# Performance work log

Hardware: AMD Instinct MI355X
Metric: run time of the kernel (lower is better)

## Reference

```python
import jax, jax.numpy as jnp
import numpy as np

B, S, E = 2, 2048, 1024
H, HKV = 16, 4
D = E // H          # head_dim = 64
REP = H // HKV      # kv repeat factor = 4


def setup_inputs() -> dict:
    key = jax.random.key(0)
    ks = jax.random.split(key, 9)
    std = 0.02
    x = jax.random.normal(ks[0], (B, S, E), dtype=jnp.float32)
    # causal mask: True means masked (upper triangle, strictly above diagonal)
    mask = jnp.triu(jnp.ones((S, S), dtype=bool), k=1)
    wq_w = jax.random.normal(ks[1], (E, E), dtype=jnp.float32) * std
    wq_b = jax.random.normal(ks[2], (E,), dtype=jnp.float32) * std
    wk_w = jax.random.normal(ks[3], (HKV * D, E), dtype=jnp.float32) * std
    wk_b = jax.random.normal(ks[4], (HKV * D,), dtype=jnp.float32) * std
    wv_w = jax.random.normal(ks[5], (HKV * D, E), dtype=jnp.float32) * std
    wv_b = jax.random.normal(ks[6], (HKV * D,), dtype=jnp.float32) * std
    wo_w = jax.random.normal(ks[7], (E, E), dtype=jnp.float32) * std
    wo_b = jax.random.normal(ks[8], (E,), dtype=jnp.float32) * std
    return {"x": x, "mask": mask, "wq_w": wq_w, "wq_b": wq_b,
            "wk_w": wk_w, "wk_b": wk_b, "wv_w": wv_w, "wv_b": wv_b,
            "wo_w": wo_w, "wo_b": wo_b}


def reference(x, mask, wq_w, wq_b, wk_w, wk_b, wv_w, wv_b, wo_w, wo_b):
    b, s, e = x.shape
    # projections (torch Linear: x @ W.T + b)
    q = x @ wq_w.T + wq_b                       # [B,S,E]
    k = x @ wk_w.T + wk_b                       # [B,S,HKV*D]
    v = x @ wv_w.T + wv_b
    # q grouped by kv head: [B, HKV, REP, S, D]; k/v: [B, HKV, S, D]
    q = q.reshape(b, s, HKV, REP, D).transpose(0, 2, 3, 1, 4)
    k = k.reshape(b, s, HKV, D).transpose(0, 2, 1, 3)
    v = v.reshape(b, s, HKV, D).transpose(0, 2, 1, 3)
    scale = D ** (-0.5)
    # scores [B, HKV, REP, Sq, Skv] -- same math as physical repeat_kv
    scores = jnp.einsum('bgrsd,bgtd->bgrst', q, k) * scale
    scores = jnp.where(mask, -jnp.inf, scores)
    w = jax.nn.softmax(scores, axis=-1)
    ctx = jnp.einsum('bgrst,bgtd->bgrsd', w, v)  # [B,HKV,REP,S,D]
    ctx = ctx.transpose(0, 3, 1, 2, 4).reshape(b, s, e)
    return ctx @ wo_w.T + wo_b
```

## Files before the change

### kernel.cpp

```cpp
#include <hip/hip_runtime.h>


typedef __attribute__((ext_vector_type(8))) short bh8;
typedef __attribute__((ext_vector_type(4))) short sh4;
typedef __attribute__((ext_vector_type(4))) float fv4;

#define MFMA16 __builtin_amdgcn_mfma_f32_16x16x32_bf16

static __device__ __forceinline__ float fast_exp2(float x) {
  return __builtin_amdgcn_exp2f(x);
}
static __device__ __forceinline__ unsigned short f2bf(float f) {
  unsigned int u; __builtin_memcpy(&u, &f, 4);
  u += 0x7fffu + ((u >> 16) & 1u);
  return (unsigned short)(u >> 16);
}
static __device__ __forceinline__ unsigned int pack2(float a, float b) {
  return (unsigned int)(unsigned short)f2bf(a) |
         ((unsigned int)(unsigned short)f2bf(b) << 16);
}
static __device__ __forceinline__ void gload16(const short* g, short* l) {
  __builtin_amdgcn_global_load_lds(
      (const __attribute__((address_space(1))) void*)g,
      (__attribute__((address_space(3))) void*)l, 16, 0, 0);
}

static __device__ __forceinline__ bh8 pshuf(const float* p, int quad, int l16) {
  unsigned int u01 = pack2(p[0], p[1]);
  unsigned int u23 = pack2(p[2], p[3]);
  unsigned int u45 = pack2(p[4], p[5]);
  unsigned int u67 = pack2(p[6], p[7]);
  const int g0 = (((quad << 1)    ) & 3) * 16 + l16;
  const int g1 = (((quad << 1) + 1) & 3) * 16 + l16;
  unsigned int w0l = __shfl((int)u01, g0), w0h = __shfl((int)u45, g0);
  unsigned int w1l = __shfl((int)u23, g0), w1h = __shfl((int)u67, g0);
  unsigned int w2l = __shfl((int)u01, g1), w2h = __shfl((int)u45, g1);
  unsigned int w3l = __shfl((int)u23, g1), w3h = __shfl((int)u67, g1);
  const bool up = (quad & 2) != 0;
  union { unsigned int w[4]; bh8 v; } pu;
  pu.w[0] = up ? w0h : w0l;
  pu.w[1] = up ? w1h : w1l;
  pu.w[2] = up ? w2h : w2l;
  pu.w[3] = up ? w3h : w3l;
  return pu.v;
}

__global__ __launch_bounds__(256) void cvt_all(
    const float* __restrict__ x,  const float* __restrict__ wq,
    const float* __restrict__ wk, const float* __restrict__ wv,
    const float* __restrict__ wo,
    short* __restrict__ xb, short* __restrict__ wqkvb, short* __restrict__ wob)
{
  const int i = blockIdx.x * 256 + threadIdx.x;
  const float* src; short* dst; int j;
  if (i < 1048576)      { j = i;           src = x;  dst = xb; }
  else if (i < 1310720) { j = i - 1048576; src = wq; dst = wqkvb; }
  else if (i < 1376256) { j = i - 1310720; src = wk; dst = wqkvb + (size_t)1024 * 1024; }
  else if (i < 1441792) { j = i - 1376256; src = wv; dst = wqkvb + (size_t)1280 * 1024; }
  else                  { j = i - 1441792; src = wo; dst = wob; }
  const float4 v = ((const float4*)src)[j];
  sh4 o = { (short)f2bf(v.x), (short)f2bf(v.y),
            (short)f2bf(v.z), (short)f2bf(v.w) };
  ((sh4*)dst)[j] = o;
}

__global__ __launch_bounds__(256) void gemm_m97(
    const short* __restrict__ A, const short* __restrict__ W,
    const float* __restrict__ biasQ, const float* __restrict__ biasK,
    const float* __restrict__ biasV,
    short* __restrict__ Cq, short* __restrict__ Ck, short* __restrict__ Cvt,
    float* __restrict__ Cf,
    int M, int K, int S, int mode, float scaleQ)
{
  __shared__ short As[128 * 64];
  __shared__ short Bs[128 * 64];
  const int tid = threadIdx.x;
  const int wave = tid >> 6, lane = tid & 63;
  const int quad = lane >> 4, l16 = lane & 15;
  const int row0 = blockIdx.x * 128, col0 = blockIdx.y * 128;
  const int wr = (wave >> 1) * 64, wc = (wave & 1) * 64;

  fv4 acc[4][4] = {};

  const int srow8  = lane >> 3;
  const int schunk = (lane & 7) ^ srow8;
  const short* agB = A + (size_t)(row0 + wave * 32 + srow8) * K + schunk * 8;
  const short* bgB = W + (size_t)(col0 + wave * 32 + srow8) * K + schunk * 8;

  const int fsw = (l16 & 7);

  for (int k0 = 0; k0 < K; k0 += 64) {
    __syncthreads();
    #pragma unroll
    for (int g = 0; g < 4; g++) {
      gload16(agB + (size_t)(g * 8) * K + k0, &As[(wave * 32 + g * 8) * 64]);
      gload16(bgB + (size_t)(g * 8) * K + k0, &Bs[(wave * 32 + g * 8) * 64]);
    }
    __syncthreads();
    #pragma unroll
    for (int ks = 0; ks < 2; ks++) {
      const int co = ((ks * 4 + quad) ^ fsw) * 8;
      bh8 af[4], bf[4];
      #pragma unroll
      for (int i = 0; i < 4; i++)
        af[i] = *(const bh8*)&As[(wr + i * 16 + l16) * 64 + co];
      #pragma unroll
      for (int j = 0; j < 4; j++)
        bf[j] = *(const bh8*)&Bs[(wc + j * 16 + l16) * 64 + co];
      #pragma unroll
      for (int i = 0; i < 4; i++)
        #pragma unroll
        for (int j = 0; j < 4; j++)
          acc[i][j] = MFMA16(af[i], bf[j], acc[i][j], 0, 0, 0);
    }
  }

  if (mode == 2) {
    float bv[4];
    #pragma unroll
    for (int j = 0; j < 4; j++) bv[j] = biasQ[col0 + wc + j * 16 + l16];
    #pragma unroll
    for (int i = 0; i < 4; i++) {
      const int row = row0 + wr + i * 16 + quad * 4;
      #pragma unroll
      for (int j = 0; j < 4; j++) {
        const int col = col0 + wc + j * 16 + l16;
        #pragma unroll
        for (int r = 0; r < 4; r++)
          Cf[(size_t)(row + r) * 1024 + col] = acc[i][j][r] + bv[j];
      }
    }
  } else if (col0 < 1024) {
    float bv[4];
    #pragma unroll
    for (int j = 0; j < 4; j++) bv[j] = biasQ[col0 + wc + j * 16 + l16];
    #pragma unroll
    for (int i = 0; i < 4; i++) {
      const int row = row0 + wr + i * 16 + quad * 4;
      #pragma unroll
      for (int j = 0; j < 4; j++) {
        const int col = col0 + wc + j * 16 + l16;
        #pragma unroll
        for (int r = 0; r < 4; r++)
          Cq[(size_t)(row + r) * 1024 + col] =
              (short)f2bf((acc[i][j][r] + bv[j]) * scaleQ);
      }
    }
  } else if (col0 < 1280) {
    float bv[4];
    #pragma unroll
    for (int j = 0; j < 4; j++) bv[j] = biasK[col0 + wc + j * 16 + l16 - 1024];
    #pragma unroll
    for (int i = 0; i < 4; i++) {
      const int row = row0 + wr + i * 16 + quad * 4;
      #pragma unroll
      for (int j = 0; j < 4; j++) {
        const int col = col0 + wc + j * 16 + l16 - 1024;
        #pragma unroll
        for (int r = 0; r < 4; r++)
          Ck[(size_t)(row + r) * 256 + col] = (short)f2bf(acc[i][j][r] + bv[j]);
      }
    }
  } else {
    float bv[4];
    #pragma unroll
    for (int j = 0; j < 4; j++) bv[j] = biasV[col0 + wc + j * 16 + l16 - 1280];
    const int b  = row0 / S;
    const int sb = row0 - b * S;
    #pragma unroll
    for (int i = 0; i < 4; i++) {
      const int s = sb + wr + i * 16 + quad * 4;
      #pragma unroll
      for (int j = 0; j < 4; j++) {
        const int np = col0 + wc + j * 16 + l16 - 1280;
        sh4 v = { (short)f2bf(acc[i][j][0] + bv[j]),
                  (short)f2bf(acc[i][j][1] + bv[j]),
                  (short)f2bf(acc[i][j][2] + bv[j]),
                  (short)f2bf(acc[i][j][3] + bv[j]) };
        *(sh4*)(Cvt + ((size_t)(b * 256 + np)) * S + s) = v;
      }
    }
  }
}

__global__ __launch_bounds__(256) void gqa_attn(
    const short* __restrict__ Q,
    const short* __restrict__ Kg,
    const short* __restrict__ Vt,
    short* __restrict__ ctx)
{
  const int S = 2048, E = 1024, KVE = 256;
  __shared__ short Ks[2][4096];
  __shared__ short Vs[2][4096];

  const int wave = threadIdx.x >> 6;
  const int lane = threadIdx.x & 63;
  const int quad = lane >> 4, l16 = lane & 15;
  const int bh = blockIdx.y;
  const int b = bh >> 4, h = bh & 15, kv = h >> 2;
  const int j = 31 - (int)blockIdx.x;
  const int qblk0 = j * 64;
  const int q0 = qblk0 + wave * 16;

  const short* Kb = Kg + (size_t)b * S * KVE + kv * 64;
  const short* Vb = Vt + ((size_t)(b * 4 + kv)) * 64 * S;

  const int srow = lane >> 3;
  const int scg  = (lane & 7) ^ srow;
  const int kc0 = (quad ^ (l16 & 7)) * 8;
  const int kc1 = ((quad ^ 4) ^ (l16 & 7)) * 8;

  auto stageKV = [&](int buf, int t0) {
    #pragma unroll
    for (int e = 0; e < 2; e++) {
      const int g = wave * 2 + e;
      const int row = g * 8 + srow;
      gload16(Kb + (size_t)(t0 + row) * KVE + scg * 8, &Ks[buf][g * 512]);
      gload16(Vb + (size_t)row * S + t0 + scg * 8,     &Vs[buf][g * 512]);
    }
  };

  const short* qrow = Q + (size_t)(b * S + q0 + l16) * E + h * 64 + quad * 8;
  bh8 qf0 = *(const bh8*)(qrow);
  bh8 qf1 = *(const bh8*)(qrow + 32);

  fv4 acc0{}, acc1{}, acc2{}, acc3{};
  float rs = 0.f;

  const int nInt = j;
  if (nInt > 0) {
    stageKV(0, 0);
    __syncthreads();
    for (int it = 0; it < nInt; it++) {
      const int cur = it & 1;
      if (it + 1 < nInt) stageKV(cur ^ 1, (it + 1) * 64);

      fv4 st[4] = {};
      #pragma unroll
      for (int i = 0; i < 4; i++) {
        const int tb = (i * 16 + l16) * 64;
        bh8 k0 = *(const bh8*)&Ks[cur][tb + kc0];
        bh8 k1 = *(const bh8*)&Ks[cur][tb + kc1];
        st[i] = MFMA16(k0, qf0, st[i], 0, 0, 0);
        st[i] = MFMA16(k1, qf1, st[i], 0, 0, 0);
      }
      float p[16];
      #pragma unroll
      for (int i = 0; i < 4; i++) {
        p[i * 4 + 0] = fast_exp2(st[i][0]);
        p[i * 4 + 1] = fast_exp2(st[i][1]);
        p[i * 4 + 2] = fast_exp2(st[i][2]);
        p[i * 4 + 3] = fast_exp2(st[i][3]);
      }
      #pragma unroll
      for (int i = 0; i < 16; i++) rs += p[i];

      bh8 pfA = pshuf(p,     quad, l16);
      bh8 pfB = pshuf(p + 8, quad, l16);
      #pragma unroll
      for (int dt = 0; dt < 4; dt++) {
        const int db = (dt * 16 + l16) * 64;
        bh8 v0 = *(const bh8*)&Vs[cur][db + kc0];
        bh8 v1 = *(const bh8*)&Vs[cur][db + kc1];
        fv4* a = dt == 0 ? &acc0 : dt == 1 ? &acc1 : dt == 2 ? &acc2 : &acc3;
        *a = MFMA16(v0, pfA, *a, 0, 0, 0);
        *a = MFMA16(v1, pfB, *a, 0, 0, 0);
      }
      __syncthreads();
    }
  }

  const int nk = q0 + 16;
  for (int t0 = qblk0; t0 < nk; t0 += 32) {
    fv4 st0{}, st1{};
    {
      const short* kr = Kb + (size_t)(t0 + l16) * KVE + quad * 8;
      bh8 k0 = *(const bh8*)(kr);
      bh8 k1 = *(const bh8*)(kr + 32);
      st0 = MFMA16(k0, qf0, st0, 0, 0, 0);
      st0 = MFMA16(k1, qf1, st0, 0, 0, 0);
    }
    const bool do2 = (t0 + 16) < nk;
    if (do2) {
      const short* kr = Kb + (size_t)(t0 + 16 + l16) * KVE + quad * 8;
      bh8 k0 = *(const bh8*)(kr);
      bh8 k1 = *(const bh8*)(kr + 32);
      st1 = MFMA16(k0, qf0, st1, 0, 0, 0);
      st1 = MFMA16(k1, qf1, st1, 0, 0, 0);
    }
    const int qg = q0 + l16;
    float p[8];
    #pragma unroll
    for (int r = 0; r < 4; r++) {
      const int t = t0 + quad * 4 + r;
      p[r]     = (t <= qg)               ? fast_exp2(st0[r]) : 0.f;
      p[4 + r] = (do2 && (t + 16) <= qg) ? fast_exp2(st1[r]) : 0.f;
    }
    #pragma unroll
    for (int i = 0; i < 8; i++) rs += p[i];

    bh8 pf = pshuf(p, quad, l16);
    const short* vr = Vb + (size_t)l16 * S + t0 + quad * 8;
    acc0 = MFMA16(*(const bh8*)(vr),          pf, acc0, 0, 0, 0);
    acc1 = MFMA16(*(const bh8*)(vr + 16 * S), pf, acc1, 0, 0, 0);
    acc2 = MFMA16(*(const bh8*)(vr + 32 * S), pf, acc2, 0, 0, 0);
    acc3 = MFMA16(*(const bh8*)(vr + 48 * S), pf, acc3, 0, 0, 0);
  }

  float lsum = rs;
  lsum += __shfl_xor(lsum, 16);
  lsum += __shfl_xor(lsum, 32);
  const float inv = 1.f / lsum;

  short* orow = ctx + (size_t)(b * S + q0 + l16) * E + h * 64 + quad * 4;
  sh4 o0 = { (short)f2bf(acc0[0] * inv), (short)f2bf(acc0[1] * inv),
             (short)f2bf(acc0[2] * inv), (short)f2bf(acc0[3] * inv) };
  sh4 o1 = { (short)f2bf(acc1[0] * inv), (short)f2bf(acc1[1] * inv),
             (short)f2bf(acc1[2] * inv), (short)f2bf(acc1[3] * inv) };
  sh4 o2 = { (short)f2bf(acc2[0] * inv), (short)f2bf(acc2[1] * inv),
             (short)f2bf(acc2[2] * inv), (short)f2bf(acc2[3] * inv) };
  sh4 o3 = { (short)f2bf(acc3[0] * inv), (short)f2bf(acc3[1] * inv),
             (short)f2bf(acc3[2] * inv), (short)f2bf(acc3[3] * inv) };
  *(sh4*)(orow)      = o0;
  *(sh4*)(orow + 16) = o1;
  *(sh4*)(orow + 32) = o2;
  *(sh4*)(orow + 48) = o3;
}

extern "C" void kernel_launch(void* const* d_in, const int* in_sizes, int n_in,
                              void* d_out, int out_size, void* d_ws, size_t ws_size,
                              hipStream_t stream)
{
  const float* x    = (const float*)d_in[0];
  const float* wq_w = (const float*)d_in[2];
  const float* wq_b = (const float*)d_in[3];
  const float* wk_w = (const float*)d_in[4];
  const float* wk_b = (const float*)d_in[5];
  const float* wv_w = (const float*)d_in[6];
  const float* wv_b = (const float*)d_in[7];
  const float* wo_w = (const float*)d_in[8];
  const float* wo_b = (const float*)d_in[9];
  float* out = (float*)d_out;

  const int S = 2048, E = 1024, M = 2 * S;
  const float sl2e = 0.125f * 1.44269504f;

  char* ob = (char*)d_out;
  short* Qb   = (short*)(ob);
  short* Kbuf = (short*)(ob + (size_t)( 8 << 20));
  short* Vtb  = (short*)(ob + (size_t)(10 << 20));

  char* ws = (char*)d_ws;
  short* xb    = (short*)(ws);
  short* wqkvb = (short*)(ws + (size_t)( 8 << 20));
  short* wob   = (short*)(ws + (size_t)(11 << 20));
  short* Cx    = xb;

  dim3 blk(256);
  cvt_all<<<dim3(6656), blk, 0, stream>>>(x, wq_w, wk_w, wv_w, wo_w,
                                          xb, wqkvb, wob);
  gemm_m97<<<dim3(M / 128, 1536 / 128), blk, 0, stream>>>(
      xb, wqkvb, wq_b, wk_b, wv_b, Qb, Kbuf, Vtb, nullptr, M, E, S, 0, sl2e);
  gqa_attn<<<dim3(32, 2 * 16), blk, 0, stream>>>(Qb, Kbuf, Vtb, Cx);
  gemm_m97<<<dim3(M / 128, 1024 / 128), blk, 0, stream>>>(
      Cx, wob, wo_b, nullptr, nullptr, nullptr, nullptr, nullptr, out,
      M, E, S, 2, 1.f);
}
```

Baseline: 206.6 us.

## Pair causal query blocks per attention CTA and shrink GEMM tiles to 64x128

Each attention block now handles two query tiles, j and 31-j, so every block does the same amount of causal work and the grid is halved to 16 blocks per head. The P probability fragments are moved from shuffles to a per-wave LDS scratch buffer for the PV MFMA. The GEMMs switch to 128-thread blocks with 64x128 tiles, doubling the block count to fill more CUs. Risks are a longer serial loop per attention block, extra LDS traffic and bank conflicts for P, and lower operand reuse in the smaller GEMM tiles.

```diff
diff --git a/kernel.cpp b/kernel.cpp
--- a/kernel.cpp
+++ b/kernel.cpp
@@ -4,6 +4,7 @@
 typedef __attribute__((ext_vector_type(8))) short bh8;
 typedef __attribute__((ext_vector_type(4))) short sh4;
 typedef __attribute__((ext_vector_type(4))) float fv4;
+typedef __attribute__((ext_vector_type(2))) unsigned int uv2;
 
 #define MFMA16 __builtin_amdgcn_mfma_f32_16x16x32_bf16
 
@@ -64,7 +65,7 @@
   ((sh4*)dst)[j] = o;
 }
 
-__global__ __launch_bounds__(256) void gemm_m97(
+__global__ __launch_bounds__(128) void gemm_2w(
     const short* __restrict__ A, const short* __restrict__ W,
     const float* __restrict__ biasQ, const float* __restrict__ biasK,
     const float* __restrict__ biasV,
@@ -72,30 +73,31 @@
     float* __restrict__ Cf,
     int M, int K, int S, int mode, float scaleQ)
 {
-  __shared__ short As[128 * 64];
+  __shared__ short As[64 * 64];
   __shared__ short Bs[128 * 64];
   const int tid = threadIdx.x;
   const int wave = tid >> 6, lane = tid & 63;
   const int quad = lane >> 4, l16 = lane & 15;
-  const int row0 = blockIdx.x * 128, col0 = blockIdx.y * 128;
-  const int wr = (wave >> 1) * 64, wc = (wave & 1) * 64;
+  const int row0 = blockIdx.x * 64, col0 = blockIdx.y * 128;
+  const int wc = wave * 64;
 
   fv4 acc[4][4] = {};
 
   const int srow8  = lane >> 3;
   const int schunk = (lane & 7) ^ srow8;
   const short* agB = A + (size_t)(row0 + wave * 32 + srow8) * K + schunk * 8;
-  const short* bgB = W + (size_t)(col0 + wave * 32 + srow8) * K + schunk * 8;
+  const short* bgB = W + (size_t)(col0 + wave * 64 + srow8) * K + schunk * 8;
 
   const int fsw = (l16 & 7);
 
   for (int k0 = 0; k0 < K; k0 += 64) {
     __syncthreads();
     #pragma unroll
-    for (int g = 0; g < 4; g++) {
+    for (int g = 0; g < 4; g++)
       gload16(agB + (size_t)(g * 8) * K + k0, &As[(wave * 32 + g * 8) * 64]);
-      gload16(bgB + (size_t)(g * 8) * K + k0, &Bs[(wave * 32 + g * 8) * 64]);
-    }
+    #pragma unroll
+    for (int g = 0; g < 8; g++)
+      gload16(bgB + (size_t)(g * 8) * K + k0, &Bs[(wave * 64 + g * 8) * 64]);
     __syncthreads();
     #pragma unroll
     for (int ks = 0; ks < 2; ks++) {
@@ -103,7 +105,7 @@
       bh8 af[4], bf[4];
       #pragma unroll
       for (int i = 0; i < 4; i++)
-        af[i] = *(const bh8*)&As[(wr + i * 16 + l16) * 64 + co];
+        af[i] = *(const bh8*)&As[(i * 16 + l16) * 64 + co];
       #pragma unroll
       for (int j = 0; j < 4; j++)
         bf[j] = *(const bh8*)&Bs[(wc + j * 16 + l16) * 64 + co];
@@ -115,47 +117,48 @@
     }
   }
 
+  const int cw0 = col0 + wc;
   if (mode == 2) {
     float bv[4];
     #pragma unroll
-    for (int j = 0; j < 4; j++) bv[j] = biasQ[col0 + wc + j * 16 + l16];
+    for (int j = 0; j < 4; j++) bv[j] = biasQ[cw0 + j * 16 + l16];
     #pragma unroll
     for (int i = 0; i < 4; i++) {
-      const int row = row0 + wr + i * 16 + quad * 4;
+      const int row = row0 + i * 16 + quad * 4;
       #pragma unroll
       for (int j = 0; j < 4; j++) {
-        const int col = col0 + wc + j * 16 + l16;
+        const int col = cw0 + j * 16 + l16;
         #pragma unroll
         for (int r = 0; r < 4; r++)
           Cf[(size_t)(row + r) * 1024 + col] = acc[i][j][r] + bv[j];
       }
     }
-  } else if (col0 < 1024) {
+  } else if (cw0 < 1024) {
     float bv[4];
     #pragma unroll
-    for (int j = 0; j < 4; j++) bv[j] = biasQ[col0 + wc + j * 16 + l16];
+    for (int j = 0; j < 4; j++) bv[j] = biasQ[cw0 + j * 16 + l16];
     #pragma unroll
     for (int i = 0; i < 4; i++) {
-      const int row = row0 + wr + i * 16 + quad * 4;
+      const int row = row0 + i * 16 + quad * 4;
       #pragma unroll
       for (int j = 0; j < 4; j++) {
-        const int col = col0 + wc + j * 16 + l16;
+        const int col = cw0 + j * 16 + l16;
         #pragma unroll
         for (int r = 0; r < 4; r++)
           Cq[(size_t)(row + r) * 1024 + col] =
               (short)f2bf((acc[i][j][r] + bv[j]) * scaleQ);
       }
     }
-  } else if (col0 < 1280) {
+  } else if (cw0 < 1280) {
     float bv[4];
     #pragma unroll
-    for (int j = 0; j < 4; j++) bv[j] = biasK[col0 + wc + j * 16 + l16 - 1024];
+    for (int j = 0; j < 4; j++) bv[j] = biasK[cw0 + j * 16 + l16 - 1024];
     #pragma unroll
     for (int i = 0; i < 4; i++) {
-      const int row = row0 + wr + i * 16 + quad * 4;
+      const int row = row0 + i * 16 + quad * 4;
       #pragma unroll
       for (int j = 0; j < 4; j++) {
-        const int col = col0 + wc + j * 16 + l16 - 1024;
+        const int col = cw0 + j * 16 + l16 - 1024;
         #pragma unroll
         for (int r = 0; r < 4; r++)
           Ck[(size_t)(row + r) * 256 + col] = (short)f2bf(acc[i][j][r] + bv[j]);
@@ -164,15 +167,15 @@
   } else {
     float bv[4];
     #pragma unroll
-    for (int j = 0; j < 4; j++) bv[j] = biasV[col0 + wc + j * 16 + l16 - 1280];
+    for (int j = 0; j < 4; j++) bv[j] = biasV[cw0 + j * 16 + l16 - 1280];
     const int b  = row0 / S;
     const int sb = row0 - b * S;
     #pragma unroll
     for (int i = 0; i < 4; i++) {
-      const int s = sb + wr + i * 16 + quad * 4;
+      const int s = sb + i * 16 + quad * 4;
       #pragma unroll
       for (int j = 0; j < 4; j++) {
-        const int np = col0 + wc + j * 16 + l16 - 1280;
+        const int np = cw0 + j * 16 + l16 - 1280;
         sh4 v = { (short)f2bf(acc[i][j][0] + bv[j]),
                   (short)f2bf(acc[i][j][1] + bv[j]),
                   (short)f2bf(acc[i][j][2] + bv[j]),
@@ -192,23 +195,24 @@
   const int S = 2048, E = 1024, KVE = 256;
   __shared__ short Ks[2][4096];
   __shared__ short Vs[2][4096];
+  __shared__ short P2[4][16 * 72];
 
   const int wave = threadIdx.x >> 6;
   const int lane = threadIdx.x & 63;
   const int quad = lane >> 4, l16 = lane & 15;
   const int bh = blockIdx.y;
   const int b = bh >> 4, h = bh & 15, kv = h >> 2;
-  const int j = 31 - (int)blockIdx.x;
-  const int qblk0 = j * 64;
-  const int q0 = qblk0 + wave * 16;
 
   const short* Kb = Kg + (size_t)b * S * KVE + kv * 64;
   const short* Vb = Vt + ((size_t)(b * 4 + kv)) * 64 * S;
+  short* Pw = &P2[wave][0];
 
   const int srow = lane >> 3;
   const int scg  = (lane & 7) ^ srow;
+
   const int kc0 = (quad ^ (l16 & 7)) * 8;
   const int kc1 = ((quad ^ 4) ^ (l16 & 7)) * 8;
+  const int pwr = l16 * 72;
 
   auto stageKV = [&](int buf, int t0) {
     #pragma unroll
@@ -220,111 +224,116 @@
     }
   };
 
-  const short* qrow = Q + (size_t)(b * S + q0 + l16) * E + h * 64 + quad * 8;
-  bh8 qf0 = *(const bh8*)(qrow);
-  bh8 qf1 = *(const bh8*)(qrow + 32);
-
-  fv4 acc0{}, acc1{}, acc2{}, acc3{};
-  float rs = 0.f;
-
-  const int nInt = j;
-  if (nInt > 0) {
-    stageKV(0, 0);
-    __syncthreads();
-    for (int it = 0; it < nInt; it++) {
-      const int cur = it & 1;
-      if (it + 1 < nInt) stageKV(cur ^ 1, (it + 1) * 64);
-
-      fv4 st[4] = {};
-      #pragma unroll
-      for (int i = 0; i < 4; i++) {
-        const int tb = (i * 16 + l16) * 64;
-        bh8 k0 = *(const bh8*)&Ks[cur][tb + kc0];
-        bh8 k1 = *(const bh8*)&Ks[cur][tb + kc1];
-        st[i] = MFMA16(k0, qf0, st[i], 0, 0, 0);
-        st[i] = MFMA16(k1, qf1, st[i], 0, 0, 0);
-      }
-      float p[16];
-      #pragma unroll
-      for (int i = 0; i < 4; i++) {
-        p[i * 4 + 0] = fast_exp2(st[i][0]);
-        p[i * 4 + 1] = fast_exp2(st[i][1]);
-        p[i * 4 + 2] = fast_exp2(st[i][2]);
-        p[i * 4 + 3] = fast_exp2(st[i][3]);
-      }
-      #pragma unroll
-      for (int i = 0; i < 16; i++) rs += p[i];
-
-      bh8 pfA = pshuf(p,     quad, l16);
-      bh8 pfB = pshuf(p + 8, quad, l16);
-      #pragma unroll
-      for (int dt = 0; dt < 4; dt++) {
-        const int db = (dt * 16 + l16) * 64;
-        bh8 v0 = *(const bh8*)&Vs[cur][db + kc0];
-        bh8 v1 = *(const bh8*)&Vs[cur][db + kc1];
-        fv4* a = dt == 0 ? &acc0 : dt == 1 ? &acc1 : dt == 2 ? &acc2 : &acc3;
-        *a = MFMA16(v0, pfA, *a, 0, 0, 0);
-        *a = MFMA16(v1, pfB, *a, 0, 0, 0);
-      }
+  for (int ph = 0; ph < 2; ph++) {
+    const int j = ph ? (31 - (int)blockIdx.x) : (int)blockIdx.x;
+    const int qblk0 = j * 64;
+    const int q0 = qblk0 + wave * 16;
+
+    const short* qrow = Q + (size_t)(b * S + q0 + l16) * E + h * 64 + quad * 8;
+    bh8 qf0 = *(const bh8*)(qrow);
+    bh8 qf1 = *(const bh8*)(qrow + 32);
+
+    fv4 acc0{}, acc1{}, acc2{}, acc3{};
+    float rs = 0.f;
+
+    const int nInt = qblk0 >> 6;
+    if (nInt > 0) {
+      stageKV(0, 0);
       __syncthreads();
-    }
+      for (int it = 0; it < nInt; it++) {
+        const int cur = it & 1;
+        if (it + 1 < nInt) stageKV(cur ^ 1, (it + 1) * 64);
+
+        fv4 st[4] = {};
+        #pragma unroll
+        for (int i = 0; i < 4; i++) {
+          const int tb = (i * 16 + l16) * 64;
+          bh8 k0 = *(const bh8*)&Ks[cur][tb + kc0];
+          bh8 k1 = *(const bh8*)&Ks[cur][tb + kc1];
+          st[i] = MFMA16(k0, qf0, st[i], 0, 0, 0);
+          st[i] = MFMA16(k1, qf1, st[i], 0, 0, 0);
+        }
+        #pragma unroll
+        for (int i = 0; i < 4; i++) {
+          float p0 = fast_exp2(st[i][0]);
+          float p1 = fast_exp2(st[i][1]);
+          float p2 = fast_exp2(st[i][2]);
+          float p3 = fast_exp2(st[i][3]);
+          rs += (p0 + p1) + (p2 + p3);
+          uv2 u = { pack2(p0, p1), pack2(p2, p3) };
+          *(uv2*)&Pw[pwr + i * 16 + quad * 4] = u;
+        }
+        bh8 pfA = *(const bh8*)&Pw[pwr + quad * 8];
+        bh8 pfB = *(const bh8*)&Pw[pwr + 32 + quad * 8];
+        #pragma unroll
+        for (int dt = 0; dt < 4; dt++) {
+          const int db = (dt * 16 + l16) * 64;
+          bh8 v0 = *(const bh8*)&Vs[cur][db + kc0];
+          bh8 v1 = *(const bh8*)&Vs[cur][db + kc1];
+          fv4* a = dt == 0 ? &acc0 : dt == 1 ? &acc1 : dt == 2 ? &acc2 : &acc3;
+          *a = MFMA16(v0, pfA, *a, 0, 0, 0);
+          *a = MFMA16(v1, pfB, *a, 0, 0, 0);
+        }
+        __syncthreads();
+      }
+    }
+
+    const int nk = q0 + 16;
+    for (int t0 = qblk0; t0 < nk; t0 += 32) {
+      fv4 st0{}, st1{};
+      {
+        const short* kr = Kb + (size_t)(t0 + l16) * KVE + quad * 8;
+        bh8 k0 = *(const bh8*)(kr);
+        bh8 k1 = *(const bh8*)(kr + 32);
+        st0 = MFMA16(k0, qf0, st0, 0, 0, 0);
+        st0 = MFMA16(k1, qf1, st0, 0, 0, 0);
+      }
+      const bool do2 = (t0 + 16) < nk;
+      if (do2) {
+        const short* kr = Kb + (size_t)(t0 + 16 + l16) * KVE + quad * 8;
+        bh8 k0 = *(const bh8*)(kr);
+        bh8 k1 = *(const bh8*)(kr + 32);
+        st1 = MFMA16(k0, qf0, st1, 0, 0, 0);
+        st1 = MFMA16(k1, qf1, st1, 0, 0, 0);
+      }
+      const int qg = q0 + l16;
+      float p[8];
+      #pragma unroll
+      for (int r = 0; r < 4; r++) {
+        const int t = t0 + quad * 4 + r;
+        p[r]     = (t <= qg)               ? fast_exp2(st0[r]) : 0.f;
+        p[4 + r] = (do2 && (t + 16) <= qg) ? fast_exp2(st1[r]) : 0.f;
+      }
+      #pragma unroll
+      for (int i = 0; i < 8; i++) rs += p[i];
+
+      bh8 pf = pshuf(p, quad, l16);
+      const short* vr = Vb + (size_t)l16 * S + t0 + quad * 8;
+      acc0 = MFMA16(*(const bh8*)(vr),          pf, acc0, 0, 0, 0);
+      acc1 = MFMA16(*(const bh8*)(vr + 16 * S), pf, acc1, 0, 0, 0);
+      acc2 = MFMA16(*(const bh8*)(vr + 32 * S), pf, acc2, 0, 0, 0);
+      acc3 = MFMA16(*(const bh8*)(vr + 48 * S), pf, acc3, 0, 0, 0);
+    }
+
+    float lsum = rs;
+    lsum += __shfl_xor(lsum, 16);
+    lsum += __shfl_xor(lsum, 32);
+    const float inv = 1.f / lsum;
+
+    short* orow = ctx + (size_t)(b * S + q0 + l16) * E + h * 64 + quad * 4;
+    sh4 o0 = { (short)f2bf(acc0[0] * inv), (short)f2bf(acc0[1] * inv),
+               (short)f2bf(acc0[2] * inv), (short)f2bf(acc0[3] * inv) };
+    sh4 o1 = { (short)f2bf(acc1[0] * inv), (short)f2bf(acc1[1] * inv),
+               (short)f2bf(acc1[2] * inv), (short)f2bf(acc1[3] * inv) };
+    sh4 o2 = { (short)f2bf(acc2[0] * inv), (short)f2bf(acc2[1] * inv),
+               (short)f2bf(acc2[2] * inv), (short)f2bf(acc2[3] * inv) };
+    sh4 o3 = { (short)f2bf(acc3[0] * inv), (short)f2bf(acc3[1] * inv),
+               (short)f2bf(acc3[2] * inv), (short)f2bf(acc3[3] * inv) };
+    *(sh4*)(orow)      = o0;
+    *(sh4*)(orow + 16) = o1;
+    *(sh4*)(orow + 32) = o2;
+    *(sh4*)(orow + 48) = o3;
   }
-
-  const int nk = q0 + 16;
-  for (int t0 = qblk0; t0 < nk; t0 += 32) {
-    fv4 st0{}, st1{};
-    {
-      const short* kr = Kb + (size_t)(t0 + l16) * KVE + quad * 8;
-      bh8 k0 = *(const bh8*)(kr);
-      bh8 k1 = *(const bh8*)(kr + 32);
-      st0 = MFMA16(k0, qf0, st0, 0, 0, 0);
-      st0 = MFMA16(k1, qf1, st0, 0, 0, 0);
-    }
-    const bool do2 = (t0 + 16) < nk;
-    if (do2) {
-      const short* kr = Kb + (size_t)(t0 + 16 + l16) * KVE + quad * 8;
-      bh8 k0 = *(const bh8*)(kr);
-      bh8 k1 = *(const bh8*)(kr + 32);
-      st1 = MFMA16(k0, qf0, st1, 0, 0, 0);
-      st1 = MFMA16(k1, qf1, st1, 0, 0, 0);
-    }
-    const int qg = q0 + l16;
-    float p[8];
-    #pragma unroll
-    for (int r = 0; r < 4; r++) {
-      const int t = t0 + quad * 4 + r;
-      p[r]     = (t <= qg)               ? fast_exp2(st0[r]) : 0.f;
-      p[4 + r] = (do2 && (t + 16) <= qg) ? fast_exp2(st1[r]) : 0.f;
-    }
-    #pragma unroll
-    for (int i = 0; i < 8; i++) rs += p[i];
-
-    bh8 pf = pshuf(p, quad, l16);
-    const short* vr = Vb + (size_t)l16 * S + t0 + quad * 8;
-    acc0 = MFMA16(*(const bh8*)(vr),          pf, acc0, 0, 0, 0);
-    acc1 = MFMA16(*(const bh8*)(vr + 16 * S), pf, acc1, 0, 0, 0);
-    acc2 = MFMA16(*(const bh8*)(vr + 32 * S), pf, acc2, 0, 0, 0);
-    acc3 = MFMA16(*(const bh8*)(vr + 48 * S), pf, acc3, 0, 0, 0);
-  }
-
-  float lsum = rs;
-  lsum += __shfl_xor(lsum, 16);
-  lsum += __shfl_xor(lsum, 32);
-  const float inv = 1.f / lsum;
-
-  short* orow = ctx + (size_t)(b * S + q0 + l16) * E + h * 64 + quad * 4;
-  sh4 o0 = { (short)f2bf(acc0[0] * inv), (short)f2bf(acc0[1] * inv),
-             (short)f2bf(acc0[2] * inv), (short)f2bf(acc0[3] * inv) };
-  sh4 o1 = { (short)f2bf(acc1[0] * inv), (short)f2bf(acc1[1] * inv),
-             (short)f2bf(acc1[2] * inv), (short)f2bf(acc1[3] * inv) };
-  sh4 o2 = { (short)f2bf(acc2[0] * inv), (short)f2bf(acc2[1] * inv),
-             (short)f2bf(acc2[2] * inv), (short)f2bf(acc2[3] * inv) };
-  sh4 o3 = { (short)f2bf(acc3[0] * inv), (short)f2bf(acc3[1] * inv),
-             (short)f2bf(acc3[2] * inv), (short)f2bf(acc3[3] * inv) };
-  *(sh4*)(orow)      = o0;
-  *(sh4*)(orow + 16) = o1;
-  *(sh4*)(orow + 32) = o2;
-  *(sh4*)(orow + 48) = o3;
 }
 
 extern "C" void kernel_launch(void* const* d_in, const int* in_sizes, int n_in,
@@ -356,13 +365,12 @@
   short* wob   = (short*)(ws + (size_t)(11 << 20));
   short* Cx    = xb;
 
-  dim3 blk(256);
-  cvt_all<<<dim3(6656), blk, 0, stream>>>(x, wq_w, wk_w, wv_w, wo_w,
-                                          xb, wqkvb, wob);
-  gemm_m97<<<dim3(M / 128, 1536 / 128), blk, 0, stream>>>(
+  cvt_all<<<dim3(6656), dim3(256), 0, stream>>>(x, wq_w, wk_w, wv_w, wo_w,
+                                                xb, wqkvb, wob);
+  gemm_2w<<<dim3(M / 64, 1536 / 128), dim3(128), 0, stream>>>(
       xb, wqkvb, wq_b, wk_b, wv_b, Qb, Kbuf, Vtb, nullptr, M, E, S, 0, sl2e);
-  gqa_attn<<<dim3(32, 2 * 16), blk, 0, stream>>>(Qb, Kbuf, Vtb, Cx);
-  gemm_m97<<<dim3(M / 128, 1024 / 128), blk, 0, stream>>>(
+  gqa_attn<<<dim3(16, 2 * 16), dim3(256), 0, stream>>>(Qb, Kbuf, Vtb, Cx);
+  gemm_2w<<<dim3(M / 64, 1024 / 128), dim3(128), 0, stream>>>(
       Cx, wob, wo_b, nullptr, nullptr, nullptr, nullptr, nullptr, out,
       M, E, S, 2, 1.f);
 }
```

Result: faster. 183.4 us (-11.2%).
